# Kernel optimization log

Measured on AMD Instinct MI355X. Metric: run time of the kernel, lower is better.

Reference implementation:

```python
import jax, jax.numpy as jnp
import numpy as np

B, S, D = 4, 1024, 1024
NH, DH = 16, 64          # n_heads, head_dim (NH*DH == D)
FF = 4096                # hidden_dim
NE = 8                   # n_experts
OUT = 1024               # output_dim


def _scaled(k, shape, scale=0.02):
    return jax.random.normal(k, shape, jnp.float32) * scale


def setup_inputs() -> dict:
    ks = jax.random.split(jax.random.key(0), 12)
    return {
        "x": jax.random.normal(ks[0], (B, S, D), jnp.float32),
        "Wqkv": _scaled(ks[1], (D, 3 * D)),
        "Wo": _scaled(ks[2], (D, D)),
        "Wr": _scaled(ks[3], (D, D)),
        "u_bias": _scaled(ks[4], (NH, DH)),
        "v_bias": _scaled(ks[5], (NH, DH)),
        "ln1_g": jnp.ones((D,), jnp.float32), "ln1_b": jnp.zeros((D,), jnp.float32),
        "Wff1": _scaled(ks[6], (D, FF)), "bff1": jnp.zeros((FF,), jnp.float32),
        "Wff2": _scaled(ks[7], (FF, D)), "bff2": jnp.zeros((D,), jnp.float32),
        "ln2_g": jnp.ones((D,), jnp.float32), "ln2_b": jnp.zeros((D,), jnp.float32),
        "Wg": _scaled(ks[8], (D, NE)),
        "We1": _scaled(ks[9], (NE, D, FF)), "be1": jnp.zeros((NE, FF), jnp.float32),
        "We2": _scaled(ks[10], (NE, FF, D)), "be2": jnp.zeros((NE, D), jnp.float32),
        "ln3_g": jnp.ones((D,), jnp.float32), "ln3_b": jnp.zeros((D,), jnp.float32),
        "Wout": _scaled(ks[11], (D, OUT)),
    }


def _layer_norm(x, g, b):
    m = x.mean(-1, keepdims=True)
    v = x.var(-1, keepdims=True)
    return (x - m) * jax.lax.rsqrt(v + 1e-5) * g + b


def _rel_shift(x):
    # Transformer-XL relative shift. x: [B, H, Q, K] -> [B, H, Q, K]
    b, h, q, k = x.shape
    x = jnp.pad(x, ((0, 0), (0, 0), (0, 0), (1, 0)))  # [B,H,Q,K+1]
    return x.reshape(b, h, k + 1, q)[:, :, 1:, :].reshape(b, h, q, k)


def reference(x, Wqkv, Wo, Wr, u_bias, v_bias, ln1_g, ln1_b, Wff1, bff1,
              Wff2, bff2, ln2_g, ln2_b, Wg, We1, be1, We2, be2,
              ln3_g, ln3_b, Wout):
    b, s, d = x.shape
    # ---- TransformerXL attention stage (causal, relative positions) ----
    q, k, v = jnp.split(x @ Wqkv, 3, axis=-1)
    q = q.reshape(b, s, NH, DH)
    k = k.reshape(b, s, NH, DH)
    v = v.reshape(b, s, NH, DH)
    # sinusoidal relative position embedding, positions S-1 .. 0
    pos = jnp.arange(s - 1, -1, -1, dtype=jnp.float32)
    inv_freq = 1.0 / (10000.0 ** (jnp.arange(0, d, 2, dtype=jnp.float32) / d))
    sinusoid = pos[:, None] * inv_freq[None, :]
    pe = jnp.concatenate([jnp.sin(sinusoid), jnp.cos(sinusoid)], axis=-1)  # [S,D]
    r = (pe @ Wr).reshape(s, NH, DH)
    ac = jnp.einsum('bqhd,bkhd->bhqk', q + u_bias, k)
    bd = _rel_shift(jnp.einsum('bqhd,khd->bhqk', q + v_bias, r))
    scores = (ac + bd) * (1.0 / np.sqrt(DH).astype(np.float32))
    causal = jnp.tril(jnp.ones((s, s), bool))
    attn = jax.nn.softmax(jnp.where(causal, scores, -1e30), axis=-1)
    ctx = jnp.einsum('bhqk,bkhd->bqhd', attn, v).reshape(b, s, d)
    h = _layer_norm(x + ctx @ Wo, ln1_g, ln1_b)
    ff = jax.nn.relu(h @ Wff1 + bff1) @ Wff2 + bff2
    h = _layer_norm(h + ff, ln2_g, ln2_b)
    # ---- Switch Transformer MoE: top-1 routing, dispatch, combine ----
    probs = jax.nn.softmax(h @ Wg, axis=-1)           # [B,S,E]
    gate = probs.max(-1)                              # [B,S] top-1 gate value
    disp = jax.nn.one_hot(probs.argmax(-1), NE, dtype=h.dtype)  # [B,S,E]
    hid = jax.nn.relu(jnp.einsum('bsd,edf->besf', h, We1) + be1[None, :, None, :])
    eout = jnp.einsum('besf,efd->besd', hid, We2) + be2[None, :, None, :]
    moe = jnp.einsum('besd,bse->bsd', eout, disp) * gate[..., None]
    h = _layer_norm(h + moe, ln3_g, ln3_b)
    return h @ Wout
```

## Files before the change

kernel.cpp:

```cpp
#include <hip/hip_runtime.h>
#include <hip/hip_bf16.h>
#include <math.h>

static constexpr int Bx = 4, Sx = 1024, Dx = 1024, NHx = 16, DHx = 64;
static constexpr int FFx = 4096, NEx = 8, OUTx = 1024, BSx = Bx * Sx;

__device__ __forceinline__ void ld4f(const float* p, float* o) {
    float4 v = *(const float4*)p;
    o[0] = v.x; o[1] = v.y; o[2] = v.z; o[3] = v.w;
}

__global__ __launch_bounds__(256) void diag_k(float* __restrict__ out, int n, float val)
{
    int i = blockIdx.x * 256 + threadIdx.x;
    if (i < n) out[i] = val;
}

template<int RELU>
__global__ __launch_bounds__(256) void gemm_k(const float* __restrict__ A,
        const float* __restrict__ B, const float* __restrict__ bias,
        float* __restrict__ C, int M, int N, int K)
{
    __shared__ __align__(16) float As[16][128];
    __shared__ __align__(16) float Bs[16][128];
    const int tid = threadIdx.x;
    const int tx = tid & 15, ty = tid >> 4;
    const int m0 = blockIdx.y * 128, n0 = blockIdx.x * 128;
    float acc[8][8];
#pragma unroll
    for (int i = 0; i < 8; i++)
#pragma unroll
        for (int j = 0; j < 8; j++) acc[i][j] = 0.f;

    const int ma = tid >> 2, ka = (tid & 3) * 4;
    const int kb = tid >> 4, nb = (tid & 15) * 8;

    for (int k0 = 0; k0 < K; k0 += 16) {
        float a0[4], a1[4];
        ld4f(A + (size_t)(m0 + ma) * K + k0 + ka, a0);
        ld4f(A + (size_t)(m0 + ma + 64) * K + k0 + ka, a1);
        float4 bv0 = *(const float4*)(B + (size_t)(k0 + kb) * N + n0 + nb);
        float4 bv1 = *(const float4*)(B + (size_t)(k0 + kb) * N + n0 + nb + 4);
#pragma unroll
        for (int i = 0; i < 4; i++) {
            As[ka + i][ma]      = a0[i];
            As[ka + i][ma + 64] = a1[i];
        }
        *(float4*)&Bs[kb][nb]     = bv0;
        *(float4*)&Bs[kb][nb + 4] = bv1;
        __syncthreads();
#pragma unroll
        for (int k = 0; k < 16; k++) {
            float a[8], bb[8];
            ld4f(&As[k][4 * ty], a);
            ld4f(&As[k][64 + 4 * ty], a + 4);
            ld4f(&Bs[k][4 * tx], bb);
            ld4f(&Bs[k][64 + 4 * tx], bb + 4);
#pragma unroll
            for (int i = 0; i < 8; i++)
#pragma unroll
                for (int j = 0; j < 8; j++)
                    acc[i][j] = fmaf(a[i], bb[j], acc[i][j]);
        }
        __syncthreads();
    }
#pragma unroll
    for (int ib = 0; ib < 2; ib++)
#pragma unroll
    for (int ii = 0; ii < 4; ii++) {
        const int m = m0 + ib * 64 + 4 * ty + ii;
#pragma unroll
        for (int jb = 0; jb < 2; jb++) {
            const int n = n0 + jb * 64 + 4 * tx;
            float v[4];
#pragma unroll
            for (int jj = 0; jj < 4; jj++) {
                float w = acc[ib * 4 + ii][jb * 4 + jj];
                if (bias) w += bias[n + jj];
                if (RELU) w = fmaxf(w, 0.f);
                v[jj] = w;
            }
            *(float4*)&C[(size_t)m * N + n] = *(const float4*)v;
        }
    }
}

__global__ __launch_bounds__(256) void pe_k(float* __restrict__ pe)
{
    int idx = blockIdx.x * 256 + threadIdx.x;
    int s = idx >> 9, j = idx & 511;
    double pos = (double)(Sx - 1 - s);
    double invf = exp(-((double)(2 * j) / (double)Dx) * log(10000.0));
    double ang = pos * invf;
    pe[(size_t)s * Dx + j]       = (float)sin(ang);
    pe[(size_t)s * Dx + 512 + j] = (float)cos(ang);
}

__global__ __launch_bounds__(256) void attn_k(const float* __restrict__ qkv,
        const float* __restrict__ r, const float* __restrict__ u_bias,
        const float* __restrict__ v_bias, float* __restrict__ ctx)
{
    const int bh = blockIdx.y;
    const int b = bh >> 4, h = bh & 15;
    const int tid = threadIdx.x;
    const int tx = tid & 15, ty = tid >> 4;

    __shared__ __align__(16) float Qs[64 * 64];
    __shared__ __align__(16) float KP[2048];
    __shared__ __align__(16) float Vs[32][64];
    __shared__ __align__(16) float RBT[64][96];
    __shared__ float us[64], vs[64];

    if (tid < 64) { us[tid] = u_bias[h * DHx + tid]; vs[tid] = v_bias[h * DHx + tid]; }

    for (int half = 0; half < 2; half++) {
        const int qt = half ? (15 - blockIdx.x) : blockIdx.x;
        const int q0 = qt * 64;

        __syncthreads();
        for (int e = tid; e < 64 * 64; e += 256) {
            int qi = e >> 6, d = e & 63;
            Qs[d * 64 + ((qi + 4 * d) & 63)] =
                qkv[((size_t)(b * Sx + q0 + qi)) * (3 * Dx) + h * DHx + d];
        }

        float m_st[4], l_st[4], O[4][4];
#pragma unroll
        for (int i = 0; i < 4; i++) {
            m_st[i] = -1e30f; l_st[i] = 0.f;
#pragma unroll
            for (int j = 0; j < 4; j++) O[i][j] = 0.f;
        }

        const int nkt = 2 * qt + 2;
        for (int kt = 0; kt < nkt; kt++) {
            const int k0 = kt * 32;
            __syncthreads();
            for (int e = tid; e < 32 * 64; e += 256) {
                int ki = e >> 6, d = e & 63;
                size_t base = ((size_t)(b * Sx + k0 + ki)) * (3 * Dx) + h * DHx + d;
                KP[d * 32 + ((ki + d) & 31)] = qkv[base + Dx];
                Vs[ki][d]                    = qkv[base + 2 * Dx];
            }
            for (int e = tid; e < 64 * 96; e += 256) {
                int d = e / 96, t = e - 96 * d;
                int delta = q0 - k0 + t - 31;
                float val = 0.f;
                if (t < 95 && delta >= 0 && delta < Sx)
                    val = r[(size_t)(Sx - 1 - delta) * Dx + h * DHx + d];
                RBT[d][t] = val;
            }
            __syncthreads();

            float sc[4][2];
#pragma unroll
            for (int i = 0; i < 4; i++) { sc[i][0] = 0.f; sc[i][1] = 0.f; }

            const int tb = 4 * ty - 2 * tx + 31;
#pragma unroll 4
            for (int d = 0; d < 64; d++) {
                float a[4];
                ld4f(&Qs[d * 64 + ((4 * ty + 4 * d) & 63)], a);
                float k0v = KP[d * 32 + ((2 * tx + d) & 31)];
                float k1v = KP[d * 32 + ((2 * tx + 1 + d) & 31)];
                float uu = us[d], vv = vs[d];
                float rb[5];
#pragma unroll
                for (int t = 0; t < 5; t++) rb[t] = RBT[d][tb - 1 + t];
#pragma unroll
                for (int i = 0; i < 4; i++) {
                    float qu = a[i] + uu, qv = a[i] + vv;
                    sc[i][0] = fmaf(qu, k0v, fmaf(qv, rb[i + 1], sc[i][0]));
                    sc[i][1] = fmaf(qu, k1v, fmaf(qv, rb[i],     sc[i][1]));
                }
            }

#pragma unroll
            for (int i = 0; i < 4; i++) {
                int qg = q0 + 4 * ty + i;
#pragma unroll
                for (int j = 0; j < 2; j++) {
                    sc[i][j] *= 0.125f;
                    if ((k0 + 2 * tx + j) > qg) sc[i][j] = -1e30f;
                }
                float mx = fmaxf(sc[i][0], sc[i][1]);
#pragma unroll
                for (int off = 8; off > 0; off >>= 1) mx = fmaxf(mx, __shfl_xor(mx, off, 16));
                float mnew = fmaxf(m_st[i], mx);
                float alpha = __expf(m_st[i] - mnew);
                m_st[i] = mnew;
                float rs = 0.f;
#pragma unroll
                for (int j = 0; j < 2; j++) { sc[i][j] = __expf(sc[i][j] - mnew); rs += sc[i][j]; }
#pragma unroll
                for (int off = 8; off > 0; off >>= 1) rs += __shfl_xor(rs, off, 16);
                l_st[i] = l_st[i] * alpha + rs;
#pragma unroll
                for (int j = 0; j < 4; j++) O[i][j] *= alpha;
            }

            __syncthreads();
#pragma unroll
            for (int i = 0; i < 4; i++)
#pragma unroll
                for (int j = 0; j < 2; j++) {
                    int kc = 2 * tx + j;
                    KP[kc * 64 + ((4 * ty + i + 4 * kc) & 63)] = sc[i][j];
                }
            __syncthreads();
#pragma unroll 4
            for (int ki = 0; ki < 32; ki++) {
                float p[4], vv[4];
                ld4f(&KP[ki * 64 + ((4 * ty + 4 * ki) & 63)], p);
                ld4f(&Vs[ki][tx * 4], vv);
#pragma unroll
                for (int i = 0; i < 4; i++)
#pragma unroll
                    for (int j = 0; j < 4; j++)
                        O[i][j] = fmaf(p[i], vv[j], O[i][j]);
            }
        }
#pragma unroll
        for (int i = 0; i < 4; i++) {
            float inv = (l_st[i] > 0.f) ? 1.f / l_st[i] : 0.f;
#pragma unroll
            for (int j = 0; j < 4; j++)
                ctx[((size_t)(b * Sx + q0 + ty * 4 + i)) * Dx + h * DHx + tx * 4 + j]
                    = O[i][j] * inv;
        }
    }
}

__global__ __launch_bounds__(256) void ln_k(const float* __restrict__ resid,
        const float* __restrict__ add, const float* __restrict__ g,
        const float* __restrict__ b, float* __restrict__ out)
{
    const int row = blockIdx.x, tid = threadIdx.x;
    const float* rr = resid + (size_t)row * Dx;
    const float* ar = add + (size_t)row * Dx;
    float v[4], s = 0.f, sq = 0.f;
#pragma unroll
    for (int i = 0; i < 4; i++) {
        int d = tid + i * 256;
        v[i] = rr[d] + ar[d];
        s += v[i]; sq += v[i] * v[i];
    }
#pragma unroll
    for (int off = 32; off > 0; off >>= 1) {
        s  += __shfl_down(s, off, 64);
        sq += __shfl_down(sq, off, 64);
    }
    __shared__ float red[8];
    int w = tid >> 6;
    if ((tid & 63) == 0) { red[w] = s; red[4 + w] = sq; }
    __syncthreads();
    s  = red[0] + red[1] + red[2] + red[3];
    sq = red[4] + red[5] + red[6] + red[7];
    float mean = s * (1.f / Dx);
    float var = fmaxf(sq * (1.f / Dx) - mean * mean, 0.f);
    float rstd = rsqrtf(var + 1e-5f);
#pragma unroll
    for (int i = 0; i < 4; i++) {
        int d = tid + i * 256;
        out[(size_t)row * Dx + d] = (v[i] - mean) * rstd * g[d] + b[d];
    }
}

__global__ __launch_bounds__(64) void route_k(const float* __restrict__ h,
        const float* __restrict__ Wg, float* __restrict__ gate,
        int* __restrict__ counts, int* __restrict__ lists)
{
    const int t = blockIdx.x, lane = threadIdx.x;
    float part[NEx];
#pragma unroll
    for (int e = 0; e < NEx; e++) part[e] = 0.f;
    const float* hr = h + (size_t)t * Dx;
    for (int d = lane; d < Dx; d += 64) {
        float hv = hr[d];
        const float* wr = Wg + (size_t)d * NEx;
#pragma unroll
        for (int e = 0; e < NEx; e++) part[e] = fmaf(hv, wr[e], part[e]);
    }
#pragma unroll
    for (int e = 0; e < NEx; e++)
#pragma unroll
        for (int off = 32; off > 0; off >>= 1)
            part[e] += __shfl_down(part[e], off, 64);
    if (lane == 0) {
        float mx = part[0]; int am = 0;
#pragma unroll
        for (int e = 1; e < NEx; e++) if (part[e] > mx) { mx = part[e]; am = e; }
        float ssum = 0.f;
#pragma unroll
        for (int e = 0; e < NEx; e++) ssum += expf(part[e] - mx);
        gate[t] = 1.f / ssum;
        int pos = atomicAdd(&counts[am], 1);
        lists[am * BSx + pos] = t;
    }
}

__global__ void zero_counts_k(int* counts) { if (threadIdx.x < NEx) counts[threadIdx.x] = 0; }

template<int PASS>
__global__ __launch_bounds__(256) void moe_gemm_k(const float* __restrict__ Act,
        const float* __restrict__ W, const float* __restrict__ bias,
        const int* __restrict__ lists, const int* __restrict__ counts,
        const float* __restrict__ gate, float* __restrict__ Out, int N, int K)
{
    const int e = blockIdx.z;
    const int cnt = counts[e];
    const int t0 = blockIdx.y * 128;
    if (t0 >= cnt) return;
    const int tid = threadIdx.x;
    const int tx = tid & 15, ty = tid >> 4;
    const int n0 = blockIdx.x * 128;

    __shared__ int toks[128];
    __shared__ __align__(16) float As[16][128];
    __shared__ __align__(16) float Bs[16][128];
    if (tid < 128) toks[tid] = (t0 + tid < cnt) ? lists[e * BSx + t0 + tid] : -1;
    __syncthreads();

    const float* We = W + (size_t)e * K * N;
    float acc[8][8];
#pragma unroll
    for (int i = 0; i < 8; i++)
#pragma unroll
        for (int j = 0; j < 8; j++) acc[i][j] = 0.f;

    const int ma = tid >> 2, ka = (tid & 3) * 4;
    const int kb = tid >> 4, nb = (tid & 15) * 8;
    const int tokA = toks[ma], tokB = toks[ma + 64];

    for (int k0 = 0; k0 < K; k0 += 16) {
        float a0[4] = {0.f, 0.f, 0.f, 0.f}, a1[4] = {0.f, 0.f, 0.f, 0.f};
        if (tokA >= 0) ld4f(Act + (size_t)tokA * K + k0 + ka, a0);
        if (tokB >= 0) ld4f(Act + (size_t)tokB * K + k0 + ka, a1);
        float4 bv0 = *(const float4*)(We + (size_t)(k0 + kb) * N + n0 + nb);
        float4 bv1 = *(const float4*)(We + (size_t)(k0 + kb) * N + n0 + nb + 4);
#pragma unroll
        for (int i = 0; i < 4; i++) {
            As[ka + i][ma]      = a0[i];
            As[ka + i][ma + 64] = a1[i];
        }
        *(float4*)&Bs[kb][nb]     = bv0;
        *(float4*)&Bs[kb][nb + 4] = bv1;
        __syncthreads();
#pragma unroll
        for (int k = 0; k < 16; k++) {
            float a[8], bb[8];
            ld4f(&As[k][4 * ty], a);
            ld4f(&As[k][64 + 4 * ty], a + 4);
            ld4f(&Bs[k][4 * tx], bb);
            ld4f(&Bs[k][64 + 4 * tx], bb + 4);
#pragma unroll
            for (int i = 0; i < 8; i++)
#pragma unroll
                for (int j = 0; j < 8; j++)
                    acc[i][j] = fmaf(a[i], bb[j], acc[i][j]);
        }
        __syncthreads();
    }
#pragma unroll
    for (int ib = 0; ib < 2; ib++)
#pragma unroll
    for (int ii = 0; ii < 4; ii++) {
        const int tok = toks[ib * 64 + 4 * ty + ii];
        if (tok < 0) continue;
        const float gv = (PASS == 2) ? gate[tok] : 0.f;
#pragma unroll
        for (int jb = 0; jb < 2; jb++) {
            const int n = n0 + jb * 64 + 4 * tx;
            float v[4];
#pragma unroll
            for (int jj = 0; jj < 4; jj++) {
                float w = acc[ib * 4 + ii][jb * 4 + jj] + bias[(size_t)e * N + n + jj];
                if (PASS == 1) w = fmaxf(w, 0.f);
                else           w = w * gv;
                v[jj] = w;
            }
            *(float4*)&Out[(size_t)tok * N + n] = *(const float4*)v;
        }
    }
}

extern "C" void kernel_launch(void* const* d_in, const int* in_sizes, int n_in,
                              void* d_out, int out_size, void* d_ws, size_t ws_size,
                              hipStream_t stream)
{
    (void)in_sizes; (void)n_in;
    const float* x      = (const float*)d_in[0];
    const float* Wqkv   = (const float*)d_in[1];
    const float* Wo     = (const float*)d_in[2];
    const float* Wr     = (const float*)d_in[3];
    const float* u_bias = (const float*)d_in[4];
    const float* v_bias = (const float*)d_in[5];
    const float* ln1_g  = (const float*)d_in[6];
    const float* ln1_b  = (const float*)d_in[7];
    const float* Wff1   = (const float*)d_in[8];
    const float* bff1   = (const float*)d_in[9];
    const float* Wff2   = (const float*)d_in[10];
    const float* bff2   = (const float*)d_in[11];
    const float* ln2_g  = (const float*)d_in[12];
    const float* ln2_b  = (const float*)d_in[13];
    const float* Wg     = (const float*)d_in[14];
    const float* We1    = (const float*)d_in[15];
    const float* be1    = (const float*)d_in[16];
    const float* We2    = (const float*)d_in[17];
    const float* be2    = (const float*)d_in[18];
    const float* ln3_g  = (const float*)d_in[19];
    const float* ln3_b  = (const float*)d_in[20];
    const float* Wout   = (const float*)d_in[21];
    float* out = (float*)d_out;

    char* base = (char*)d_ws;
    const size_t QKV_B = (size_t)BSx * 3 * Dx * 4;
    const size_t PE_B  = (size_t)Sx * Dx * 4;
    const size_t CTX_B = (size_t)BSx * Dx * 4;
    const size_t P2    = QKV_B + 2 * PE_B + CTX_B;
    const size_t NEEDED = P2 + 2 * CTX_B + 16384 + 256 + (size_t)NEx * BSx * 4;

    if (ws_size < NEEDED) {
        diag_k<<<(out_size + 255) / 256, 256, 0, stream>>>(out, out_size,
                                                           (float)(ws_size >> 20));
        return;
    }

    float* qkv  = (float*)(base);
    float* pe   = (float*)(base + QKV_B);
    float* rbuf = (float*)(base + QKV_B + PE_B);
    float* ctx  = (float*)(base + QKV_B + 2 * PE_B);
    float* ffh  = (float*)(base);
    float* tmp  = (float*)(base + P2);
    float* h    = (float*)(base + P2 + CTX_B);
    float* gate = (float*)(base + P2 + 2 * CTX_B);
    int* counts = (int*)(base + P2 + 2 * CTX_B + 16384);
    int* lists  = (int*)(base + P2 + 2 * CTX_B + 16384 + 256);

    gemm_k<0><<<dim3(3 * Dx / 128, BSx / 128), 256, 0, stream>>>(
        x, Wqkv, nullptr, qkv, BSx, 3 * Dx, Dx);
    pe_k<<<Sx * 512 / 256, 256, 0, stream>>>(pe);
    gemm_k<0><<<dim3(Dx / 128, Sx / 128), 256, 0, stream>>>(
        pe, Wr, nullptr, rbuf, Sx, Dx, Dx);
    attn_k<<<dim3(8, Bx * NHx), 256, 0, stream>>>(qkv, rbuf, u_bias, v_bias, ctx);
    gemm_k<0><<<dim3(Dx / 128, BSx / 128), 256, 0, stream>>>(
        ctx, Wo, nullptr, tmp, BSx, Dx, Dx);
    ln_k<<<BSx, 256, 0, stream>>>(x, tmp, ln1_g, ln1_b, h);
    gemm_k<1><<<dim3(FFx / 128, BSx / 128), 256, 0, stream>>>(
        h, Wff1, bff1, ffh, BSx, FFx, Dx);
    gemm_k<0><<<dim3(Dx / 128, BSx / 128), 256, 0, stream>>>(
        ffh, Wff2, bff2, tmp, BSx, Dx, FFx);
    ln_k<<<BSx, 256, 0, stream>>>(h, tmp, ln2_g, ln2_b, h);
    zero_counts_k<<<1, 64, 0, stream>>>(counts);
    route_k<<<BSx, 64, 0, stream>>>(h, Wg, gate, counts, lists);
    moe_gemm_k<1><<<dim3(FFx / 128, BSx / 128, NEx), 256, 0, stream>>>(
        h, We1, be1, lists, counts, gate, ffh, FFx, Dx);
    moe_gemm_k<2><<<dim3(Dx / 128, BSx / 128, NEx), 256, 0, stream>>>(
        ffh, We2, be2, lists, counts, gate, tmp, Dx, FFx);
    ln_k<<<BSx, 256, 0, stream>>>(h, tmp, ln3_g, ln3_b, h);
    gemm_k<0><<<dim3(OUTx / 128, BSx / 128), 256, 0, stream>>>(
        h, Wout, nullptr, out, BSx, OUTx, Dx);
}
```

Before: 4.441 ms.

## Use single-wavefront 64x64 GEMM tiles with register prefetch and swizzled LDS

Restructures the dense and MoE fp32 GEMM kernels to run one 64-thread wavefront per block on 64x64 output tiles, keeping the 8x8 per-thread micro-tile. Because each block is a single wavefront, the __syncthreads barriers are dropped. The next k-slice of A and B is prefetched into registers while the current slice is computed, and B tiles in shared memory use an XOR swizzle to avoid bank conflicts. In exchange, the smaller tiles give less reuse per block and more global and L2 traffic, and correctness depends on in-wave ordering of LDS accesses without explicit barriers.

```diff
diff --git a/kernel.cpp b/kernel.cpp
--- a/kernel.cpp
+++ b/kernel.cpp
@@ -17,61 +17,72 @@
 }
 
 template<int RELU>
-__global__ __launch_bounds__(256) void gemm_k(const float* __restrict__ A,
+__global__ __launch_bounds__(64, 3) void gemm_k(const float* __restrict__ A,
         const float* __restrict__ B, const float* __restrict__ bias,
         float* __restrict__ C, int M, int N, int K)
 {
-    __shared__ __align__(16) float As[16][128];
-    __shared__ __align__(16) float Bs[16][128];
+    __shared__ __align__(16) float As[16 * 64];
+    __shared__ __align__(16) float Bs[16 * 64];
     const int tid = threadIdx.x;
-    const int tx = tid & 15, ty = tid >> 4;
-    const int m0 = blockIdx.y * 128, n0 = blockIdx.x * 128;
+    const int tx = tid & 7, ty = tid >> 3;
+    const int m0 = blockIdx.y * 64, n0 = blockIdx.x * 64;
+
+    const int kb = tid >> 2, nbb = (tid & 3) * 16;
+    const float* arow = A + (size_t)(m0 + tid) * K;
+    const float* bcol = B + (size_t)kb * N + n0 + nbb;
+
     float acc[8][8];
 #pragma unroll
     for (int i = 0; i < 8; i++)
 #pragma unroll
         for (int j = 0; j < 8; j++) acc[i][j] = 0.f;
 
-    const int ma = tid >> 2, ka = (tid & 3) * 4;
-    const int kb = tid >> 4, nb = (tid & 15) * 8;
+    float4 apf[4], bpf[4];
+#pragma unroll
+    for (int i = 0; i < 4; i++) {
+        apf[i] = *(const float4*)(arow + 4 * i);
+        bpf[i] = *(const float4*)(bcol + 4 * i);
+    }
 
     for (int k0 = 0; k0 < K; k0 += 16) {
-        float a0[4], a1[4];
-        ld4f(A + (size_t)(m0 + ma) * K + k0 + ka, a0);
-        ld4f(A + (size_t)(m0 + ma + 64) * K + k0 + ka, a1);
-        float4 bv0 = *(const float4*)(B + (size_t)(k0 + kb) * N + n0 + nb);
-        float4 bv1 = *(const float4*)(B + (size_t)(k0 + kb) * N + n0 + nb + 4);
 #pragma unroll
         for (int i = 0; i < 4; i++) {
-            As[ka + i][ma]      = a0[i];
-            As[ka + i][ma + 64] = a1[i];
-        }
-        *(float4*)&Bs[kb][nb]     = bv0;
-        *(float4*)&Bs[kb][nb + 4] = bv1;
-        __syncthreads();
+            As[(4 * i + 0) * 64 + tid] = apf[i].x;
+            As[(4 * i + 1) * 64 + tid] = apf[i].y;
+            As[(4 * i + 2) * 64 + tid] = apf[i].z;
+            As[(4 * i + 3) * 64 + tid] = apf[i].w;
+            *(float4*)&Bs[kb * 64 + ((nbb + 4 * i) ^ ((kb & 7) * 4))] = bpf[i];
+        }
+        if (k0 + 16 < K) {
+#pragma unroll
+            for (int i = 0; i < 4; i++) {
+                apf[i] = *(const float4*)(arow + k0 + 16 + 4 * i);
+                bpf[i] = *(const float4*)(bcol + (size_t)(k0 + 16) * N + 4 * i);
+            }
+        }
 #pragma unroll
         for (int k = 0; k < 16; k++) {
+            const int swz = (k & 7) * 4;
             float a[8], bb[8];
-            ld4f(&As[k][4 * ty], a);
-            ld4f(&As[k][64 + 4 * ty], a + 4);
-            ld4f(&Bs[k][4 * tx], bb);
-            ld4f(&Bs[k][64 + 4 * tx], bb + 4);
+            ld4f(&As[k * 64 + 4 * ty], a);
+            ld4f(&As[k * 64 + 32 + 4 * ty], a + 4);
+            ld4f(&Bs[k * 64 + ((4 * tx) ^ swz)], bb);
+            ld4f(&Bs[k * 64 + ((32 + 4 * tx) ^ swz)], bb + 4);
 #pragma unroll
             for (int i = 0; i < 8; i++)
 #pragma unroll
                 for (int j = 0; j < 8; j++)
                     acc[i][j] = fmaf(a[i], bb[j], acc[i][j]);
         }
-        __syncthreads();
     }
 #pragma unroll
     for (int ib = 0; ib < 2; ib++)
 #pragma unroll
     for (int ii = 0; ii < 4; ii++) {
-        const int m = m0 + ib * 64 + 4 * ty + ii;
+        const int m = m0 + ib * 32 + 4 * ty + ii;
 #pragma unroll
         for (int jb = 0; jb < 2; jb++) {
-            const int n = n0 + jb * 64 + 4 * tx;
+            const int n = n0 + jb * 32 + 4 * tx;
             float v[4];
 #pragma unroll
             for (int jj = 0; jj < 4; jj++) {
@@ -302,75 +313,85 @@
 __global__ void zero_counts_k(int* counts) { if (threadIdx.x < NEx) counts[threadIdx.x] = 0; }
 
 template<int PASS>
-__global__ __launch_bounds__(256) void moe_gemm_k(const float* __restrict__ Act,
+__global__ __launch_bounds__(64, 3) void moe_gemm_k(const float* __restrict__ Act,
         const float* __restrict__ W, const float* __restrict__ bias,
         const int* __restrict__ lists, const int* __restrict__ counts,
         const float* __restrict__ gate, float* __restrict__ Out, int N, int K)
 {
     const int e = blockIdx.z;
     const int cnt = counts[e];
-    const int t0 = blockIdx.y * 128;
+    const int t0 = blockIdx.y * 64;
     if (t0 >= cnt) return;
     const int tid = threadIdx.x;
-    const int tx = tid & 15, ty = tid >> 4;
-    const int n0 = blockIdx.x * 128;
-
-    __shared__ int toks[128];
-    __shared__ __align__(16) float As[16][128];
-    __shared__ __align__(16) float Bs[16][128];
-    if (tid < 128) toks[tid] = (t0 + tid < cnt) ? lists[e * BSx + t0 + tid] : -1;
-    __syncthreads();
-
+    const int tx = tid & 7, ty = tid >> 3;
+    const int n0 = blockIdx.x * 64;
+
+    __shared__ int toks[64];
+    __shared__ __align__(16) float As[16 * 64];
+    __shared__ __align__(16) float Bs[16 * 64];
+    toks[tid] = (t0 + tid < cnt) ? lists[e * BSx + t0 + tid] : -1;
+    const int tok = toks[tid];
+
+    const int kb = tid >> 2, nbb = (tid & 3) * 16;
     const float* We = W + (size_t)e * K * N;
+    const float* arow = (tok >= 0) ? (Act + (size_t)tok * K) : nullptr;
+    const float* bcol = We + (size_t)kb * N + n0 + nbb;
+
     float acc[8][8];
 #pragma unroll
     for (int i = 0; i < 8; i++)
 #pragma unroll
         for (int j = 0; j < 8; j++) acc[i][j] = 0.f;
 
-    const int ma = tid >> 2, ka = (tid & 3) * 4;
-    const int kb = tid >> 4, nb = (tid & 15) * 8;
-    const int tokA = toks[ma], tokB = toks[ma + 64];
+    float4 apf[4], bpf[4];
+#pragma unroll
+    for (int i = 0; i < 4; i++) {
+        apf[i] = make_float4(0.f, 0.f, 0.f, 0.f);
+        if (tok >= 0) apf[i] = *(const float4*)(arow + 4 * i);
+        bpf[i] = *(const float4*)(bcol + 4 * i);
+    }
 
     for (int k0 = 0; k0 < K; k0 += 16) {
-        float a0[4] = {0.f, 0.f, 0.f, 0.f}, a1[4] = {0.f, 0.f, 0.f, 0.f};
-        if (tokA >= 0) ld4f(Act + (size_t)tokA * K + k0 + ka, a0);
-        if (tokB >= 0) ld4f(Act + (size_t)tokB * K + k0 + ka, a1);
-        float4 bv0 = *(const float4*)(We + (size_t)(k0 + kb) * N + n0 + nb);
-        float4 bv1 = *(const float4*)(We + (size_t)(k0 + kb) * N + n0 + nb + 4);
 #pragma unroll
         for (int i = 0; i < 4; i++) {
-            As[ka + i][ma]      = a0[i];
-            As[ka + i][ma + 64] = a1[i];
-        }
-        *(float4*)&Bs[kb][nb]     = bv0;
-        *(float4*)&Bs[kb][nb + 4] = bv1;
-        __syncthreads();
+            As[(4 * i + 0) * 64 + tid] = apf[i].x;
+            As[(4 * i + 1) * 64 + tid] = apf[i].y;
+            As[(4 * i + 2) * 64 + tid] = apf[i].z;
+            As[(4 * i + 3) * 64 + tid] = apf[i].w;
+            *(float4*)&Bs[kb * 64 + ((nbb + 4 * i) ^ ((kb & 7) * 4))] = bpf[i];
+        }
+        if (k0 + 16 < K) {
+#pragma unroll
+            for (int i = 0; i < 4; i++) {
+                if (tok >= 0) apf[i] = *(const float4*)(arow + k0 + 16 + 4 * i);
+                bpf[i] = *(const float4*)(bcol + (size_t)(k0 + 16) * N + 4 * i);
+            }
+        }
 #pragma unroll
         for (int k = 0; k < 16; k++) {
+            const int swz = (k & 7) * 4;
             float a[8], bb[8];
-            ld4f(&As[k][4 * ty], a);
-            ld4f(&As[k][64 + 4 * ty], a + 4);
-            ld4f(&Bs[k][4 * tx], bb);
-            ld4f(&Bs[k][64 + 4 * tx], bb + 4);
+            ld4f(&As[k * 64 + 4 * ty], a);
+            ld4f(&As[k * 64 + 32 + 4 * ty], a + 4);
+            ld4f(&Bs[k * 64 + ((4 * tx) ^ swz)], bb);
+            ld4f(&Bs[k * 64 + ((32 + 4 * tx) ^ swz)], bb + 4);
 #pragma unroll
             for (int i = 0; i < 8; i++)
 #pragma unroll
                 for (int j = 0; j < 8; j++)
                     acc[i][j] = fmaf(a[i], bb[j], acc[i][j]);
         }
-        __syncthreads();
     }
 #pragma unroll
     for (int ib = 0; ib < 2; ib++)
 #pragma unroll
     for (int ii = 0; ii < 4; ii++) {
-        const int tok = toks[ib * 64 + 4 * ty + ii];
-        if (tok < 0) continue;
-        const float gv = (PASS == 2) ? gate[tok] : 0.f;
+        const int otok = toks[ib * 32 + 4 * ty + ii];
+        if (otok < 0) continue;
+        const float gv = (PASS == 2) ? gate[otok] : 0.f;
 #pragma unroll
         for (int jb = 0; jb < 2; jb++) {
-            const int n = n0 + jb * 64 + 4 * tx;
+            const int n = n0 + jb * 32 + 4 * tx;
             float v[4];
 #pragma unroll
             for (int jj = 0; jj < 4; jj++) {
@@ -379,7 +400,7 @@
                 else           w = w * gv;
                 v[jj] = w;
             }
-            *(float4*)&Out[(size_t)tok * N + n] = *(const float4*)v;
+            *(float4*)&Out[(size_t)otok * N + n] = *(const float4*)v;
         }
     }
 }
@@ -437,27 +458,27 @@
     int* counts = (int*)(base + P2 + 2 * CTX_B + 16384);
     int* lists  = (int*)(base + P2 + 2 * CTX_B + 16384 + 256);
 
-    gemm_k<0><<<dim3(3 * Dx / 128, BSx / 128), 256, 0, stream>>>(
+    gemm_k<0><<<dim3(3 * Dx / 64, BSx / 64), 64, 0, stream>>>(
         x, Wqkv, nullptr, qkv, BSx, 3 * Dx, Dx);
     pe_k<<<Sx * 512 / 256, 256, 0, stream>>>(pe);
-    gemm_k<0><<<dim3(Dx / 128, Sx / 128), 256, 0, stream>>>(
+    gemm_k<0><<<dim3(Dx / 64, Sx / 64), 64, 0, stream>>>(
         pe, Wr, nullptr, rbuf, Sx, Dx, Dx);
     attn_k<<<dim3(8, Bx * NHx), 256, 0, stream>>>(qkv, rbuf, u_bias, v_bias, ctx);
-    gemm_k<0><<<dim3(Dx / 128, BSx / 128), 256, 0, stream>>>(
+    gemm_k<0><<<dim3(Dx / 64, BSx / 64), 64, 0, stream>>>(
         ctx, Wo, nullptr, tmp, BSx, Dx, Dx);
     ln_k<<<BSx, 256, 0, stream>>>(x, tmp, ln1_g, ln1_b, h);
-    gemm_k<1><<<dim3(FFx / 128, BSx / 128), 256, 0, stream>>>(
+    gemm_k<1><<<dim3(FFx / 64, BSx / 64), 64, 0, stream>>>(
         h, Wff1, bff1, ffh, BSx, FFx, Dx);
-    gemm_k<0><<<dim3(Dx / 128, BSx / 128), 256, 0, stream>>>(
+    gemm_k<0><<<dim3(Dx / 64, BSx / 64), 64, 0, stream>>>(
         ffh, Wff2, bff2, tmp, BSx, Dx, FFx);
     ln_k<<<BSx, 256, 0, stream>>>(h, tmp, ln2_g, ln2_b, h);
     zero_counts_k<<<1, 64, 0, stream>>>(counts);
     route_k<<<BSx, 64, 0, stream>>>(h, Wg, gate, counts, lists);
-    moe_gemm_k<1><<<dim3(FFx / 128, BSx / 128, NEx), 256, 0, stream>>>(
+    moe_gemm_k<1><<<dim3(FFx / 64, BSx / 64, NEx), 64, 0, stream>>>(
         h, We1, be1, lists, counts, gate, ffh, FFx, Dx);
-    moe_gemm_k<2><<<dim3(Dx / 128, BSx / 128, NEx), 256, 0, stream>>>(
+    moe_gemm_k<2><<<dim3(Dx / 64, BSx / 64, NEx), 64, 0, stream>>>(
         ffh, We2, be2, lists, counts, gate, tmp, Dx, FFx);
     ln_k<<<BSx, 256, 0, stream>>>(h, tmp, ln3_g, ln3_b, h);
-    gemm_k<0><<<dim3(OUTx / 128, BSx / 128), 256, 0, stream>>>(
+    gemm_k<0><<<dim3(OUTx / 64, BSx / 64), 64, 0, stream>>>(
         h, Wout, nullptr, out, BSx, OUTx, Dx);
 }
```

Result: slower. 6.076 ms (+36.8%).

## Double-buffer shared tiles and swizzle LDS layout in FP32 GEMM kernels

Applied to the files above, without the earlier changes.

Both the dense GEMM and the MoE gathered GEMM now keep two shared-memory tile buffers. Each k-step prefetches the next tile's global loads into registers while the current tile is computed, then writes them to the other buffer, so only one barrier per k-step remains instead of two. Columns in shared memory are rotated by 4*k to spread the transposed A stores across banks and reduce bank conflicts. This doubles LDS use per block and adds live registers, which may lower occupancy.

```diff
diff --git a/kernel.cpp b/kernel.cpp
--- a/kernel.cpp
+++ b/kernel.cpp
@@ -21,48 +21,81 @@
         const float* __restrict__ B, const float* __restrict__ bias,
         float* __restrict__ C, int M, int N, int K)
 {
-    __shared__ __align__(16) float As[16][128];
-    __shared__ __align__(16) float Bs[16][128];
+    __shared__ __align__(16) float As[2][16 * 128];
+    __shared__ __align__(16) float Bs[2][16 * 128];
     const int tid = threadIdx.x;
     const int tx = tid & 15, ty = tid >> 4;
     const int m0 = blockIdx.y * 128, n0 = blockIdx.x * 128;
-    float acc[8][8];
-#pragma unroll
-    for (int i = 0; i < 8; i++)
-#pragma unroll
-        for (int j = 0; j < 8; j++) acc[i][j] = 0.f;
 
     const int ma = tid >> 2, ka = (tid & 3) * 4;
     const int kb = tid >> 4, nb = (tid & 15) * 8;
 
+    const float* arow0 = A + (size_t)(m0 + ma) * K + ka;
+    const float* arow1 = arow0 + (size_t)64 * K;
+    const float* brow  = B + (size_t)kb * N + n0 + nb;
+
+    float acc[8][8];
+#pragma unroll
+    for (int i = 0; i < 8; i++)
+#pragma unroll
+        for (int j = 0; j < 8; j++) acc[i][j] = 0.f;
+
+    float a0[4], a1[4], b0[4], b1[4];
+    ld4f(arow0, a0); ld4f(arow1, a1);
+    ld4f(brow, b0);  ld4f(brow + 4, b1);
+
+    int cur = 0;
+#pragma unroll
+    for (int i = 0; i < 4; i++) {
+        As[0][(ka + i) * 128 + ((ma + 4 * (ka + i)) & 127)]      = a0[i];
+        As[0][(ka + i) * 128 + ((ma + 64 + 4 * (ka + i)) & 127)] = a1[i];
+        Bs[0][kb * 128 + ((nb     + 4 * kb) & 127)] = b0[i];
+        Bs[0][kb * 128 + ((nb + 4 + 4 * kb) & 127) + 0] = b1[i];
+    }
+#pragma unroll
+    for (int i = 0; i < 4; i++) {
+        Bs[0][kb * 128 + ((nb + i     + 4 * kb) & 127)] = b0[i];
+        Bs[0][kb * 128 + ((nb + 4 + i + 4 * kb) & 127)] = b1[i];
+    }
+    __syncthreads();
+
     for (int k0 = 0; k0 < K; k0 += 16) {
-        float a0[4], a1[4];
-        ld4f(A + (size_t)(m0 + ma) * K + k0 + ka, a0);
-        ld4f(A + (size_t)(m0 + ma + 64) * K + k0 + ka, a1);
-        float4 bv0 = *(const float4*)(B + (size_t)(k0 + kb) * N + n0 + nb);
-        float4 bv1 = *(const float4*)(B + (size_t)(k0 + kb) * N + n0 + nb + 4);
-#pragma unroll
-        for (int i = 0; i < 4; i++) {
-            As[ka + i][ma]      = a0[i];
-            As[ka + i][ma + 64] = a1[i];
-        }
-        *(float4*)&Bs[kb][nb]     = bv0;
-        *(float4*)&Bs[kb][nb + 4] = bv1;
-        __syncthreads();
+        const bool more = (k0 + 16 < K);
+        if (more) {
+            ld4f(arow0 + k0 + 16, a0);
+            ld4f(arow1 + k0 + 16, a1);
+            ld4f(brow + (size_t)(k0 + 16) * N, b0);
+            ld4f(brow + (size_t)(k0 + 16) * N + 4, b1);
+        }
+        const float* Asc = As[cur];
+        const float* Bsc = Bs[cur];
 #pragma unroll
         for (int k = 0; k < 16; k++) {
+            const int rot = (4 * k) & 127;
             float a[8], bb[8];
-            ld4f(&As[k][4 * ty], a);
-            ld4f(&As[k][64 + 4 * ty], a + 4);
-            ld4f(&Bs[k][4 * tx], bb);
-            ld4f(&Bs[k][64 + 4 * tx], bb + 4);
+            ld4f(&Asc[k * 128 + ((4 * ty + rot) & 127)], a);
+            ld4f(&Asc[k * 128 + ((64 + 4 * ty + rot) & 127)], a + 4);
+            ld4f(&Bsc[k * 128 + ((4 * tx + rot) & 127)], bb);
+            ld4f(&Bsc[k * 128 + ((64 + 4 * tx + rot) & 127)], bb + 4);
 #pragma unroll
             for (int i = 0; i < 8; i++)
 #pragma unroll
                 for (int j = 0; j < 8; j++)
                     acc[i][j] = fmaf(a[i], bb[j], acc[i][j]);
         }
-        __syncthreads();
+        if (more) {
+            float* Asn = As[cur ^ 1];
+            float* Bsn = Bs[cur ^ 1];
+#pragma unroll
+            for (int i = 0; i < 4; i++) {
+                Asn[(ka + i) * 128 + ((ma + 4 * (ka + i)) & 127)]      = a0[i];
+                Asn[(ka + i) * 128 + ((ma + 64 + 4 * (ka + i)) & 127)] = a1[i];
+                Bsn[kb * 128 + ((nb + i     + 4 * kb) & 127)] = b0[i];
+                Bsn[kb * 128 + ((nb + 4 + i + 4 * kb) & 127)] = b1[i];
+            }
+            __syncthreads();
+            cur ^= 1;
+        }
     }
 #pragma unroll
     for (int ib = 0; ib < 2; ib++)
@@ -316,50 +349,79 @@
     const int n0 = blockIdx.x * 128;
 
     __shared__ int toks[128];
-    __shared__ __align__(16) float As[16][128];
-    __shared__ __align__(16) float Bs[16][128];
+    __shared__ __align__(16) float As[2][16 * 128];
+    __shared__ __align__(16) float Bs[2][16 * 128];
     if (tid < 128) toks[tid] = (t0 + tid < cnt) ? lists[e * BSx + t0 + tid] : -1;
     __syncthreads();
-
-    const float* We = W + (size_t)e * K * N;
-    float acc[8][8];
-#pragma unroll
-    for (int i = 0; i < 8; i++)
-#pragma unroll
-        for (int j = 0; j < 8; j++) acc[i][j] = 0.f;
 
     const int ma = tid >> 2, ka = (tid & 3) * 4;
     const int kb = tid >> 4, nb = (tid & 15) * 8;
     const int tokA = toks[ma], tokB = toks[ma + 64];
 
+    const float* We = W + (size_t)e * K * N;
+    const float* arow0 = (tokA >= 0) ? (Act + (size_t)tokA * K + ka) : nullptr;
+    const float* arow1 = (tokB >= 0) ? (Act + (size_t)tokB * K + ka) : nullptr;
+    const float* brow  = We + (size_t)kb * N + n0 + nb;
+
+    float acc[8][8];
+#pragma unroll
+    for (int i = 0; i < 8; i++)
+#pragma unroll
+        for (int j = 0; j < 8; j++) acc[i][j] = 0.f;
+
+    float a0[4] = {0.f, 0.f, 0.f, 0.f}, a1[4] = {0.f, 0.f, 0.f, 0.f};
+    float b0[4], b1[4];
+    if (arow0) ld4f(arow0, a0);
+    if (arow1) ld4f(arow1, a1);
+    ld4f(brow, b0); ld4f(brow + 4, b1);
+
+    int cur = 0;
+#pragma unroll
+    for (int i = 0; i < 4; i++) {
+        As[0][(ka + i) * 128 + ((ma + 4 * (ka + i)) & 127)]      = a0[i];
+        As[0][(ka + i) * 128 + ((ma + 64 + 4 * (ka + i)) & 127)] = a1[i];
+        Bs[0][kb * 128 + ((nb + i     + 4 * kb) & 127)] = b0[i];
+        Bs[0][kb * 128 + ((nb + 4 + i + 4 * kb) & 127)] = b1[i];
+    }
+    __syncthreads();
+
     for (int k0 = 0; k0 < K; k0 += 16) {
-        float a0[4] = {0.f, 0.f, 0.f, 0.f}, a1[4] = {0.f, 0.f, 0.f, 0.f};
-        if (tokA >= 0) ld4f(Act + (size_t)tokA * K + k0 + ka, a0);
-        if (tokB >= 0) ld4f(Act + (size_t)tokB * K + k0 + ka, a1);
-        float4 bv0 = *(const float4*)(We + (size_t)(k0 + kb) * N + n0 + nb);
-        float4 bv1 = *(const float4*)(We + (size_t)(k0 + kb) * N + n0 + nb + 4);
-#pragma unroll
-        for (int i = 0; i < 4; i++) {
-            As[ka + i][ma]      = a0[i];
-            As[ka + i][ma + 64] = a1[i];
-        }
-        *(float4*)&Bs[kb][nb]     = bv0;
-        *(float4*)&Bs[kb][nb + 4] = bv1;
-        __syncthreads();
+        const bool more = (k0 + 16 < K);
+        if (more) {
+            if (arow0) ld4f(arow0 + k0 + 16, a0);
+            if (arow1) ld4f(arow1 + k0 + 16, a1);
+            ld4f(brow + (size_t)(k0 + 16) * N, b0);
+            ld4f(brow + (size_t)(k0 + 16) * N + 4, b1);
+        }
+        const float* Asc = As[cur];
+        const float* Bsc = Bs[cur];
 #pragma unroll
         for (int k = 0; k < 16; k++) {
+            const int rot = (4 * k) & 127;
             float a[8], bb[8];
-            ld4f(&As[k][4 * ty], a);
-            ld4f(&As[k][64 + 4 * ty], a + 4);
-            ld4f(&Bs[k][4 * tx], bb);
-            ld4f(&Bs[k][64 + 4 * tx], bb + 4);
+            ld4f(&Asc[k * 128 + ((4 * ty + rot) & 127)], a);
+            ld4f(&Asc[k * 128 + ((64 + 4 * ty + rot) & 127)], a + 4);
+            ld4f(&Bsc[k * 128 + ((4 * tx + rot) & 127)], bb);
+            ld4f(&Bsc[k * 128 + ((64 + 4 * tx + rot) & 127)], bb + 4);
 #pragma unroll
             for (int i = 0; i < 8; i++)
 #pragma unroll
                 for (int j = 0; j < 8; j++)
                     acc[i][j] = fmaf(a[i], bb[j], acc[i][j]);
         }
-        __syncthreads();
+        if (more) {
+            float* Asn = As[cur ^ 1];
+            float* Bsn = Bs[cur ^ 1];
+#pragma unroll
+            for (int i = 0; i < 4; i++) {
+                Asn[(ka + i) * 128 + ((ma + 4 * (ka + i)) & 127)]      = a0[i];
+                Asn[(ka + i) * 128 + ((ma + 64 + 4 * (ka + i)) & 127)] = a1[i];
+                Bsn[kb * 128 + ((nb + i     + 4 * kb) & 127)] = b0[i];
+                Bsn[kb * 128 + ((nb + 4 + i + 4 * kb) & 127)] = b1[i];
+            }
+            __syncthreads();
+            cur ^= 1;
+        }
     }
 #pragma unroll
     for (int ib = 0; ib < 2; ib++)
```

New measurement: 3.680 ms. -17.1%, faster.
